# Optimization experiments

Hardware: AMD Instinct MI355X
Metric: run time of the kernel (lower is better)

Reference implementation:

```python
import jax, jax.numpy as jnp
import numpy as np

B, C, T = 8, 256, 8192
CALC, H = 256, 4
D = CALC // H  # head dim = 64
EPS = 1e-5


def setup_inputs() -> dict:
    key = jax.random.key(0)
    ks = jax.random.split(key, 5)
    return {
        "x": jax.random.normal(ks[0], (B, C, T), dtype=jnp.float32),
        "W_prenet": jax.random.normal(ks[1], (3 * CALC, C), dtype=jnp.float32) * 0.05,
        "W_proj": jax.random.normal(ks[2], (C, CALC), dtype=jnp.float32) * 0.05,
        "b_proj": jax.random.normal(ks[3], (C,), dtype=jnp.float32) * 0.05,
        "scale": jax.random.normal(ks[4], (1,), dtype=jnp.float32),
        "gamma": jnp.ones((C,), dtype=jnp.float32),
        "beta": jnp.zeros((C,), dtype=jnp.float32),
    }


def reference(x, W_prenet, W_proj, b_proj, scale, gamma, beta):
    residual = x
    # 1x1 conv prenet: [B, 3*CALC, T]
    h = jnp.einsum('oc,bct->bot', W_prenet, x)
    # split heads: channels grouped as H blocks of 3*D, then chunk into q/k/v of D each
    h = h.reshape(B, H, 3 * D, T)
    q = h[:, :, :D, :]            # [B,H,D,T]
    k = h[:, :, D:2 * D, :]
    v = h[:, :, 2 * D:, :]
    # softmax over time on keys (with the module's +1e-5 shift)
    k = jax.nn.softmax(k + EPS, axis=3)
    # keys @ values^T : [B,H,Dk,Dv]
    kv = jnp.einsum('bhdt,bhet->bhde', k, v)
    # kv^T @ queries  : [B,H,Dv,T]
    ctx = jnp.einsum('bhde,bhdt->bhet', kv, q)
    ctx = ctx.reshape(B, CALC, T)
    # 1x1 conv projection + bias
    out = jnp.einsum('oc,bct->bot', W_proj, ctx) + b_proj[None, :, None]
    out = scale * out  # learnable scalar gate
    # dropout is identity in eval mode
    out = out + residual
    # LayerNorm over channel axis with per-channel affine
    mean = jnp.mean(out, axis=1, keepdims=True)
    var = jnp.var(out, axis=1, keepdims=True)
    out = (out - mean) * jax.lax.rsqrt(var + EPS)
    out = out * gamma[None, :, None] + beta[None, :, None]
    return out
```

## Files before the change

### kernel.cpp

```cpp
#include <hip/hip_runtime.h>
#include <hip/hip_bf16.h>
#include <math.h>

#define BB 8
#define CC 256
#define TT 8192
#define EPSF 1e-5f

typedef short v8s __attribute__((ext_vector_type(8)));
typedef float v4f __attribute__((ext_vector_type(4)));

#define MFMA(a, b, c) __builtin_amdgcn_mfma_f32_16x16x32_bf16((a), (b), (c), 0, 0, 0)


#define OFF_WKV 0
#define OFF_WPJ 65536
#define OFF_UPART 98304
#define OFF_ZPART 4292608
#define OFF_KV 4423680
#define OFF_PT 4554752
#define OFF_MBF 4816896

__device__ __forceinline__ unsigned short f2bf(float f) {
  __hip_bfloat16 h = __float2bfloat16(f);
  return __builtin_bit_cast(unsigned short, h);
}
__device__ __forceinline__ float bf2f(unsigned short u) {
  return __bfloat162float(__builtin_bit_cast(__hip_bfloat16, u));
}
__device__ __forceinline__ unsigned int pack2(float lo, float hi) {
  return (unsigned int)f2bf(lo) | ((unsigned int)f2bf(hi) << 16);
}

__global__ void k0_pack(const float* __restrict__ Wpre,
                        const float* __restrict__ Wproj,
                        float* __restrict__ ws) {
  const int r = blockIdx.x;
  const int c = threadIdx.x;
  if (r < 512) {
    const int h = r >> 7, type = (r >> 6) & 1, d = r & 63;
    const int src = h * 192 + 64 + type * 64 + d;
    ((unsigned short*)(ws + OFF_WKV))[r * 256 + c] = f2bf(Wpre[(size_t)src * 256 + c]);
  } else {
    const int rr = r - 512;
    ((unsigned short*)(ws + OFF_WPJ))[rr * 256 + c] = f2bf(Wproj[(size_t)rr * 256 + c]);
  }
}

__global__ __launch_bounds__(512, 1) void k1_kv(const float* __restrict__ x,
                                                float* __restrict__ ws) {
  __shared__ unsigned short lds[74752];

  const int tid = threadIdx.x;
  const int w = tid >> 6, lane = tid & 63, q = lane >> 4, cl = lane & 15;
  const int h = w >> 1, thalf = w & 1;
  const int tw0 = thalf * 32;
  const int bi = blockIdx.x;
  const int b = bi >> 5, chunk = bi & 31;
  const int t0 = chunk * 256;
  const float* xb = x + (size_t)b * (CC * TT);
  const unsigned short* wk =
      (const unsigned short*)(ws + OFF_WKV) + (size_t)((h * 2 + 0) * 64) * 256;
  const unsigned short* wv =
      (const unsigned short*)(ws + OFF_WKV) + (size_t)((h * 2 + 1) * 64) * 256;
  unsigned short* evh = &lds[33792 + (h * 2) * 5120];
  unsigned short* ekw = evh + thalf * 5120;
  unsigned short* vbw = ekw + 2560;

  v4f Uacc[2][4];
#pragma unroll
  for (int i = 0; i < 2; ++i)
#pragma unroll
    for (int j = 0; j < 4; ++j) Uacc[i][j] = (v4f){0.f, 0.f, 0.f, 0.f};
  float zacc[4][4];
#pragma unroll
  for (int i = 0; i < 4; ++i)
#pragma unroll
    for (int j = 0; j < 4; ++j) zacc[i][j] = 0.f;

  const int c0 = (tid & 127) * 2;
  const int th = tid >> 7;
  const int cw = tid & 127;
  unsigned int* l32 = (unsigned int*)lds;

  {
    const float* xpA = xb + (size_t)c0 * TT + t0 + th * 16;
    const float* xpB = xpA + TT;
#pragma unroll
    for (int k = 0; k < 4; ++k) {
      const float4 va = reinterpret_cast<const float4*>(xpA)[k];
      const float4 vb4 = reinterpret_cast<const float4*>(xpB)[k];
      const int tb = th * 16 + k * 4;
      l32[(tb + 0) * 132 + cw] = pack2(va.x, vb4.x);
      l32[(tb + 1) * 132 + cw] = pack2(va.y, vb4.y);
      l32[(tb + 2) * 132 + cw] = pack2(va.z, vb4.z);
      l32[(tb + 3) * 132 + cw] = pack2(va.w, vb4.w);
    }
  }

  for (int sub = 0; sub < 4; ++sub) {
    const int cur = sub & 1;
    const unsigned short* xsr = &lds[cur * 16896];
    __syncthreads();

    v4f acc[4][2];

#pragma unroll
    for (int i = 0; i < 4; ++i)
#pragma unroll
      for (int j = 0; j < 2; ++j) acc[i][j] = (v4f){0.f, 0.f, 0.f, 0.f};
#pragma unroll
    for (int ks = 0; ks < 8; ++ks) {
      v8s af[4], bfu[2];
#pragma unroll
      for (int rt = 0; rt < 4; ++rt)
        af[rt] = *(const v8s*)(wk + (size_t)(rt * 16 + cl) * 256 + ks * 32 + q * 8);
#pragma unroll
      for (int ct = 0; ct < 2; ++ct)
        bfu[ct] = *(const v8s*)&xsr[(tw0 + ct * 16 + cl) * 264 + ks * 32 + q * 8];
#pragma unroll
      for (int rt = 0; rt < 4; ++rt)
#pragma unroll
        for (int ct = 0; ct < 2; ++ct)
          acc[rt][ct] = MFMA(af[rt], bfu[ct], acc[rt][ct]);
    }
#pragma unroll
    for (int rt = 0; rt < 4; ++rt)
#pragma unroll
      for (int ct = 0; ct < 2; ++ct)
#pragma unroll
        for (int reg = 0; reg < 4; ++reg) {
          const int row = rt * 16 + q * 4 + reg;
          const float e = __expf(acc[rt][ct][reg]);
          zacc[rt][reg] += e;
          ekw[row * 40 + ct * 16 + cl] = f2bf(e);
        }

#pragma unroll
    for (int i = 0; i < 4; ++i)
#pragma unroll
      for (int j = 0; j < 2; ++j) acc[i][j] = (v4f){0.f, 0.f, 0.f, 0.f};
#pragma unroll
    for (int ks = 0; ks < 8; ++ks) {
      v8s af[4], bfu[2];
#pragma unroll
      for (int rt = 0; rt < 4; ++rt)
        af[rt] = *(const v8s*)(wv + (size_t)(rt * 16 + cl) * 256 + ks * 32 + q * 8);
#pragma unroll
      for (int ct = 0; ct < 2; ++ct)
        bfu[ct] = *(const v8s*)&xsr[(tw0 + ct * 16 + cl) * 264 + ks * 32 + q * 8];
#pragma unroll
      for (int rt = 0; rt < 4; ++rt)
#pragma unroll
        for (int ct = 0; ct < 2; ++ct)
          acc[rt][ct] = MFMA(af[rt], bfu[ct], acc[rt][ct]);
    }
#pragma unroll
    for (int rt = 0; rt < 4; ++rt)
#pragma unroll
      for (int ct = 0; ct < 2; ++ct)
#pragma unroll
        for (int reg = 0; reg < 4; ++reg) {
          const int row = rt * 16 + q * 4 + reg;
          vbw[row * 40 + ct * 16 + cl] = f2bf(acc[rt][ct][reg]);
        }
    __syncthreads();

    float4 nxA[4], nxB[4];
    if (sub < 3) {
      const float* xpA = xb + (size_t)c0 * TT + (t0 + (sub + 1) * 64) + th * 16;
      const float* xpB = xpA + TT;
#pragma unroll
      for (int k = 0; k < 4; ++k) {
        nxA[k] = reinterpret_cast<const float4*>(xpA)[k];
        nxB[k] = reinterpret_cast<const float4*>(xpB)[k];
      }
    }

#pragma unroll
    for (int s = 0; s < 2; ++s) {
      const unsigned short* eks = evh + s * 5120;
      const unsigned short* vbs = eks + 2560;
      v8s afu[2], bfv[4];
#pragma unroll
      for (int ur = 0; ur < 2; ++ur)
        afu[ur] = *(const v8s*)&eks[(tw0 + ur * 16 + cl) * 40 + q * 8];
#pragma unroll
      for (int uc = 0; uc < 4; ++uc)
        bfv[uc] = *(const v8s*)&vbs[(uc * 16 + cl) * 40 + q * 8];
#pragma unroll
      for (int ur = 0; ur < 2; ++ur)
#pragma unroll
        for (int uc = 0; uc < 4; ++uc)
          Uacc[ur][uc] = MFMA(afu[ur], bfv[uc], Uacc[ur][uc]);
    }

    if (sub < 3) {
      unsigned int* xw = l32 + (cur ^ 1) * 8448;
#pragma unroll
      for (int k = 0; k < 4; ++k) {
        const int tb = th * 16 + k * 4;
        xw[(tb + 0) * 132 + cw] = pack2(nxA[k].x, nxB[k].x);
        xw[(tb + 1) * 132 + cw] = pack2(nxA[k].y, nxB[k].y);
        xw[(tb + 2) * 132 + cw] = pack2(nxA[k].z, nxB[k].z);
        xw[(tb + 3) * 132 + cw] = pack2(nxA[k].w, nxB[k].w);
      }
    }
  }

#pragma unroll
  for (int m = 1; m < 16; m <<= 1)
#pragma unroll
    for (int rt = 0; rt < 4; ++rt)
#pragma unroll
      for (int reg = 0; reg < 4; ++reg)
        zacc[rt][reg] += __shfl_xor(zacc[rt][reg], m, 64);
  if (cl == 0) {
    for (int rt = 0; rt < 4; ++rt)
      for (int reg = 0; reg < 4; ++reg)
        ws[OFF_ZPART + (size_t)bi * 512 + w * 64 + rt * 16 + q * 4 + reg] =
            zacc[rt][reg];
  }
  float* Up = ws + OFF_UPART + (size_t)bi * 16384 + h * 4096;
#pragma unroll
  for (int ur = 0; ur < 2; ++ur)
#pragma unroll
    for (int uc = 0; uc < 4; ++uc)
#pragma unroll
      for (int reg = 0; reg < 4; ++reg)
        Up[(tw0 + ur * 16 + q * 4 + reg) * 64 + uc * 16 + cl] =
            Uacc[ur][uc][reg];
}

__global__ void k2_reduce_kv(float* __restrict__ ws) {
  const int bi = blockIdx.x;
  const int bh = bi >> 4, j = bi & 15;
  const int b = bh >> 2, h = bh & 3;
  const int tid = threadIdx.x;

  __shared__ float zinv[64];
  if (tid < 64) {
    float z = 0.f;
#pragma unroll 4
    for (int cb = 0; cb < 32; ++cb) {
      const size_t base = OFF_ZPART + (size_t)(b * 32 + cb) * 512;
      z += ws[base + (h * 2 + 0) * 64 + tid] + ws[base + (h * 2 + 1) * 64 + tid];
    }
    zinv[tid] = 1.0f / z;
  }
  __syncthreads();

  const int idx = j * 256 + tid;
  const int d = idx >> 6;
  float s = 0.f;
#pragma unroll 4
  for (int cb = 0; cb < 32; ++cb)
    s += ws[OFF_UPART + (size_t)(b * 32 + cb) * 16384 + h * 4096 + idx];
  ws[OFF_KV + (size_t)(b * 4 + h) * 4096 + idx] = s * zinv[d];
}

__global__ void k3a_P(const float* __restrict__ Wpre, float* __restrict__ ws) {
  const int bi = blockIdx.x;
  const int b = bi >> 8, he = bi & 255;
  const int h = he >> 6, e = he & 63;
  const int c = threadIdx.x;
  const float* kvp = ws + OFF_KV + (size_t)(b * 4 + h) * 4096;
  float acc = 0.f;
#pragma unroll 8
  for (int d = 0; d < 64; ++d)
    acc += kvp[d * 64 + e] * Wpre[(size_t)(h * 192 + d) * 256 + c];
  ((unsigned short*)(ws + OFF_PT))[(size_t)b * 65536 + (size_t)c * 256 + he] =
      f2bf(acc);
}

__global__ __launch_bounds__(256, 2) void k3b_M(const float* __restrict__ scale,
                                                float* __restrict__ ws) {
  const int bi = blockIdx.x;
  const int b = bi >> 4, cg = (bi >> 2) & 3, rg = bi & 3;
  const int tid = threadIdx.x, w = tid >> 6, lane = tid & 63, q = lane >> 4,
            cl = lane & 15;
  const unsigned short* wpj = (const unsigned short*)(ws + OFF_WPJ);
  const unsigned short* pt =
      (const unsigned short*)(ws + OFF_PT) + (size_t)b * 65536;
  v4f acc[4];
#pragma unroll
  for (int j = 0; j < 4; ++j) acc[j] = (v4f){0.f, 0.f, 0.f, 0.f};
#pragma unroll
  for (int ks = 0; ks < 8; ++ks) {
    const v8s af = *(const v8s*)(wpj + (size_t)(rg * 64 + w * 16 + cl) * 256 +
                                 ks * 32 + q * 8);
    v8s bfu[4];
#pragma unroll
    for (int ct = 0; ct < 4; ++ct)
      bfu[ct] = *(const v8s*)(pt + (size_t)(cg * 64 + ct * 16 + cl) * 256 +
                              ks * 32 + q * 8);
#pragma unroll
    for (int ct = 0; ct < 4; ++ct) acc[ct] = MFMA(af, bfu[ct], acc[ct]);
  }
  const float s = scale[0];
  unsigned short* mbf = (unsigned short*)(ws + OFF_MBF);
#pragma unroll
  for (int ct = 0; ct < 4; ++ct)
#pragma unroll
    for (int reg = 0; reg < 4; ++reg) {
      const int o = rg * 64 + w * 16 + q * 4 + reg;
      const int c = cg * 64 + ct * 16 + cl;
      mbf[((size_t)b * 256 + o) * 256 + c] = f2bf(s * acc[ct][reg]);
    }
}

__global__ __launch_bounds__(256, 2) void k4_proj_ln(
    const float* __restrict__ x, const float* __restrict__ bproj,
    const float* __restrict__ scale, const float* __restrict__ gamma,
    const float* __restrict__ beta, const float* __restrict__ ws,
    float* __restrict__ out) {
  __shared__ unsigned short xs[32 * 264];
  __shared__ float red1[128], red2[128], muA[32], rsA[32];
  const int bi = blockIdx.x, b = bi >> 8, tc = bi & 255;
  const int tg0 = tc * 32;
  const int tid = threadIdx.x, w = tid >> 6, lane = tid & 63, q = lane >> 4,
            cl = lane & 15;
  const float* xb = x + (size_t)b * (CC * TT);

  {
    const int c0 = (tid & 127) * 2;
    const int th = tid >> 7;
    const float* xpA = xb + (size_t)c0 * TT + tg0 + th * 16;
    const float* xpB = xpA + TT;
    unsigned int* x32 = (unsigned int*)xs;
    const int cw = c0 >> 1;
#pragma unroll
    for (int k = 0; k < 4; ++k) {
      const float4 va = reinterpret_cast<const float4*>(xpA)[k];
      const float4 vb = reinterpret_cast<const float4*>(xpB)[k];
      const int tb = th * 16 + k * 4;
      x32[(tb + 0) * 132 + cw] = pack2(va.x, vb.x);
      x32[(tb + 1) * 132 + cw] = pack2(va.y, vb.y);
      x32[(tb + 2) * 132 + cw] = pack2(va.z, vb.z);
      x32[(tb + 3) * 132 + cw] = pack2(va.w, vb.w);
    }
  }
  __syncthreads();

  const unsigned short* mbf =
      (const unsigned short*)(ws + OFF_MBF) + (size_t)b * 65536;
  v4f acc[4][2];
#pragma unroll
  for (int i = 0; i < 4; ++i)
#pragma unroll
    for (int j = 0; j < 2; ++j) acc[i][j] = (v4f){0.f, 0.f, 0.f, 0.f};
#pragma unroll
  for (int ks = 0; ks < 8; ++ks) {
    v8s af[4], bfu[2];
#pragma unroll
    for (int rt = 0; rt < 4; ++rt)
      af[rt] = *(const v8s*)(mbf + (size_t)(w * 64 + rt * 16 + cl) * 256 +
                             ks * 32 + q * 8);
#pragma unroll
    for (int ct = 0; ct < 2; ++ct)
      bfu[ct] = *(const v8s*)&xs[(ct * 16 + cl) * 264 + ks * 32 + q * 8];
#pragma unroll
    for (int rt = 0; rt < 4; ++rt)
#pragma unroll
      for (int ct = 0; ct < 2; ++ct)
        acc[rt][ct] = MFMA(af[rt], bfu[ct], acc[rt][ct]);
  }

  const float s = scale[0];
#pragma unroll
  for (int rt = 0; rt < 4; ++rt)
#pragma unroll
    for (int reg = 0; reg < 4; ++reg) {
      const int o = w * 64 + rt * 16 + q * 4 + reg;
      const float sb = s * bproj[o];
#pragma unroll
      for (int ct = 0; ct < 2; ++ct) {
        const int tl = ct * 16 + cl;
        acc[rt][ct][reg] += sb + bf2f(xs[tl * 264 + o]);
      }
    }

#pragma unroll
  for (int ct = 0; ct < 2; ++ct) {
    float s1 = 0.f, s2 = 0.f;
#pragma unroll
    for (int rt = 0; rt < 4; ++rt)
#pragma unroll
      for (int reg = 0; reg < 4; ++reg) {
        const float v = acc[rt][ct][reg];
        s1 += v;
        s2 += v * v;
      }
    s1 += __shfl_xor(s1, 16, 64);
    s1 += __shfl_xor(s1, 32, 64);
    s2 += __shfl_xor(s2, 16, 64);
    s2 += __shfl_xor(s2, 32, 64);
    if (q == 0) {
      red1[w * 32 + ct * 16 + cl] = s1;
      red2[w * 32 + ct * 16 + cl] = s2;
    }
  }
  __syncthreads();
  if (tid < 32) {
    const float s1 = red1[tid] + red1[32 + tid] + red1[64 + tid] + red1[96 + tid];
    const float s2 = red2[tid] + red2[32 + tid] + red2[64 + tid] + red2[96 + tid];
    const float mu = s1 * (1.f / 256.f);
    const float var = s2 * (1.f / 256.f) - mu * mu;
    muA[tid] = mu;
    rsA[tid] = rsqrtf(var + EPSF);
  }
  __syncthreads();

  float* ob = out + (size_t)b * (CC * TT) + tg0;
#pragma unroll
  for (int rt = 0; rt < 4; ++rt)
#pragma unroll
    for (int reg = 0; reg < 4; ++reg) {
      const int o = w * 64 + rt * 16 + q * 4 + reg;
      const float g = gamma[o], bt = beta[o];
#pragma unroll
      for (int ct = 0; ct < 2; ++ct) {
        const int tl = ct * 16 + cl;
        ob[(size_t)o * TT + tl] = (acc[rt][ct][reg] - muA[tl]) * rsA[tl] * g + bt;
      }
    }
}

extern "C" void kernel_launch(void* const* d_in, const int* in_sizes, int n_in,
                              void* d_out, int out_size, void* d_ws,
                              size_t ws_size, hipStream_t stream) {
  (void)in_sizes; (void)n_in; (void)out_size; (void)ws_size;
  const float* x = (const float*)d_in[0];
  const float* Wpre = (const float*)d_in[1];
  const float* Wproj = (const float*)d_in[2];
  const float* bproj = (const float*)d_in[3];
  const float* scale = (const float*)d_in[4];
  const float* gamma = (const float*)d_in[5];
  const float* beta = (const float*)d_in[6];
  float* out = (float*)d_out;
  float* ws = (float*)d_ws;

  hipLaunchKernelGGL(k0_pack, dim3(768), dim3(256), 0, stream, Wpre, Wproj, ws);
  hipLaunchKernelGGL(k1_kv, dim3(256), dim3(512), 0, stream, x, ws);
  hipLaunchKernelGGL(k2_reduce_kv, dim3(512), dim3(256), 0, stream, ws);
  hipLaunchKernelGGL(k3a_P, dim3(BB * 256), dim3(256), 0, stream, Wpre, ws);
  hipLaunchKernelGGL(k3b_M, dim3(128), dim3(256), 0, stream, scale, ws);
  hipLaunchKernelGGL(k4_proj_ln, dim3(BB * 128 * 2), dim3(256), 0, stream, x,
                     bproj, scale, gamma, beta, ws, out);
}
```

Baseline: 254.1 us.

## Halve k1 time chunk and shrink LDS to fit two blocks per CU

The kv-accumulation kernel now processes 128 time steps per block instead of 256, launching 512 blocks. LDS drops from about 146KB to 65KB by removing x double-buffering and packing the exp(k) and v tiles into a dense 32-column XOR-swizzled layout, which also targets bank conflicts. Launch bounds allow two blocks per CU. In exchange it adds barriers, gives up the x double-buffer overlap, and doubles the partial sums the reduce kernel must read, with workspace offsets moved to fit.

```diff
diff --git a/kernel.cpp b/kernel.cpp
--- a/kernel.cpp
+++ b/kernel.cpp
@@ -16,10 +16,10 @@
 #define OFF_WKV 0
 #define OFF_WPJ 65536
 #define OFF_UPART 98304
-#define OFF_ZPART 4292608
-#define OFF_KV 4423680
-#define OFF_PT 4554752
-#define OFF_MBF 4816896
+#define OFF_ZPART 8486912
+#define OFF_KV 8749056
+#define OFF_PT 8880128
+#define OFF_MBF 9142272
 
 __device__ __forceinline__ unsigned short f2bf(float f) {
   __hip_bfloat16 h = __float2bfloat16(f);
@@ -30,6 +30,13 @@
 }
 __device__ __forceinline__ unsigned int pack2(float lo, float hi) {
   return (unsigned int)f2bf(lo) | ((unsigned int)f2bf(hi) << 16);
+}
+__device__ __forceinline__ int swz_w(int row, int col) {
+  return row * 32 + ((((col >> 3) ^ (row & 3) ^ ((row >> 2) & 3)) & 3) << 3) +
+         (col & 7);
+}
+__device__ __forceinline__ int swz_r(int row, int q) {
+  return row * 32 + (((q ^ (row & 3) ^ ((row >> 2) & 3)) & 3) << 3);
 }
 
 __global__ void k0_pack(const float* __restrict__ Wpre,
@@ -47,25 +54,24 @@
   }
 }
 
-__global__ __launch_bounds__(512, 1) void k1_kv(const float* __restrict__ x,
+__global__ __launch_bounds__(512, 2) void k1_kv(const float* __restrict__ x,
                                                 float* __restrict__ ws) {
-  __shared__ unsigned short lds[74752];
+  __shared__ unsigned short lds[33280];
 
   const int tid = threadIdx.x;
   const int w = tid >> 6, lane = tid & 63, q = lane >> 4, cl = lane & 15;
   const int h = w >> 1, thalf = w & 1;
   const int tw0 = thalf * 32;
   const int bi = blockIdx.x;
-  const int b = bi >> 5, chunk = bi & 31;
-  const int t0 = chunk * 256;
+  const int b = bi >> 6, chunk = bi & 63;
+  const int t0 = chunk * 128;
   const float* xb = x + (size_t)b * (CC * TT);
   const unsigned short* wk =
       (const unsigned short*)(ws + OFF_WKV) + (size_t)((h * 2 + 0) * 64) * 256;
   const unsigned short* wv =
       (const unsigned short*)(ws + OFF_WKV) + (size_t)((h * 2 + 1) * 64) * 256;
-  unsigned short* evh = &lds[33792 + (h * 2) * 5120];
-  unsigned short* ekw = evh + thalf * 5120;
-  unsigned short* vbw = ekw + 2560;
+  unsigned short* ekw = &lds[16896 + h * 4096 + thalf * 2048];
+  unsigned short* vbw_ = &lds[h * 4096 + thalf * 2048];
 
   v4f Uacc[2][4];
 #pragma unroll
@@ -98,9 +104,7 @@
     }
   }
 
-  for (int sub = 0; sub < 4; ++sub) {
-    const int cur = sub & 1;
-    const unsigned short* xsr = &lds[cur * 16896];
+  for (int sub = 0; sub < 2; ++sub) {
     __syncthreads();
 
     v4f acc[4][2];
@@ -117,7 +121,7 @@
         af[rt] = *(const v8s*)(wk + (size_t)(rt * 16 + cl) * 256 + ks * 32 + q * 8);
 #pragma unroll
       for (int ct = 0; ct < 2; ++ct)
-        bfu[ct] = *(const v8s*)&xsr[(tw0 + ct * 16 + cl) * 264 + ks * 32 + q * 8];
+        bfu[ct] = *(const v8s*)&lds[(tw0 + ct * 16 + cl) * 264 + ks * 32 + q * 8];
 #pragma unroll
       for (int rt = 0; rt < 4; ++rt)
 #pragma unroll
@@ -133,7 +137,7 @@
           const int row = rt * 16 + q * 4 + reg;
           const float e = __expf(acc[rt][ct][reg]);
           zacc[rt][reg] += e;
-          ekw[row * 40 + ct * 16 + cl] = f2bf(e);
+          ekw[swz_w(row, ct * 16 + cl)] = f2bf(e);
         }
 
 #pragma unroll
@@ -148,13 +152,15 @@
         af[rt] = *(const v8s*)(wv + (size_t)(rt * 16 + cl) * 256 + ks * 32 + q * 8);
 #pragma unroll
       for (int ct = 0; ct < 2; ++ct)
-        bfu[ct] = *(const v8s*)&xsr[(tw0 + ct * 16 + cl) * 264 + ks * 32 + q * 8];
+        bfu[ct] = *(const v8s*)&lds[(tw0 + ct * 16 + cl) * 264 + ks * 32 + q * 8];
 #pragma unroll
       for (int rt = 0; rt < 4; ++rt)
 #pragma unroll
         for (int ct = 0; ct < 2; ++ct)
           acc[rt][ct] = MFMA(af[rt], bfu[ct], acc[rt][ct]);
     }
+    __syncthreads();
+
 #pragma unroll
     for (int rt = 0; rt < 4; ++rt)
 #pragma unroll
@@ -162,13 +168,12 @@
 #pragma unroll
         for (int reg = 0; reg < 4; ++reg) {
           const int row = rt * 16 + q * 4 + reg;
-          vbw[row * 40 + ct * 16 + cl] = f2bf(acc[rt][ct][reg]);
+          vbw_[swz_w(row, ct * 16 + cl)] = f2bf(acc[rt][ct][reg]);
         }
-    __syncthreads();
 
     float4 nxA[4], nxB[4];
-    if (sub < 3) {
-      const float* xpA = xb + (size_t)c0 * TT + (t0 + (sub + 1) * 64) + th * 16;
+    if (sub == 0) {
+      const float* xpA = xb + (size_t)c0 * TT + (t0 + 64) + th * 16;
       const float* xpB = xpA + TT;
 #pragma unroll
       for (int k = 0; k < 4; ++k) {
@@ -176,18 +181,19 @@
         nxB[k] = reinterpret_cast<const float4*>(xpB)[k];
       }
     }
+    __syncthreads();
 
 #pragma unroll
     for (int s = 0; s < 2; ++s) {
-      const unsigned short* eks = evh + s * 5120;
-      const unsigned short* vbs = eks + 2560;
+      const unsigned short* eks = &lds[16896 + h * 4096 + s * 2048];
+      const unsigned short* vbs = &lds[h * 4096 + s * 2048];
       v8s afu[2], bfv[4];
 #pragma unroll
       for (int ur = 0; ur < 2; ++ur)
-        afu[ur] = *(const v8s*)&eks[(tw0 + ur * 16 + cl) * 40 + q * 8];
+        afu[ur] = *(const v8s*)&eks[swz_r(tw0 + ur * 16 + cl, q)];
 #pragma unroll
       for (int uc = 0; uc < 4; ++uc)
-        bfv[uc] = *(const v8s*)&vbs[(uc * 16 + cl) * 40 + q * 8];
+        bfv[uc] = *(const v8s*)&vbs[swz_r(uc * 16 + cl, q)];
 #pragma unroll
       for (int ur = 0; ur < 2; ++ur)
 #pragma unroll
@@ -195,15 +201,15 @@
           Uacc[ur][uc] = MFMA(afu[ur], bfv[uc], Uacc[ur][uc]);
     }
 
-    if (sub < 3) {
-      unsigned int* xw = l32 + (cur ^ 1) * 8448;
+    if (sub == 0) {
+      __syncthreads();
 #pragma unroll
       for (int k = 0; k < 4; ++k) {
         const int tb = th * 16 + k * 4;
-        xw[(tb + 0) * 132 + cw] = pack2(nxA[k].x, nxB[k].x);
-        xw[(tb + 1) * 132 + cw] = pack2(nxA[k].y, nxB[k].y);
-        xw[(tb + 2) * 132 + cw] = pack2(nxA[k].z, nxB[k].z);
-        xw[(tb + 3) * 132 + cw] = pack2(nxA[k].w, nxB[k].w);
+        l32[(tb + 0) * 132 + cw] = pack2(nxA[k].x, nxB[k].x);
+        l32[(tb + 1) * 132 + cw] = pack2(nxA[k].y, nxB[k].y);
+        l32[(tb + 2) * 132 + cw] = pack2(nxA[k].z, nxB[k].z);
+        l32[(tb + 3) * 132 + cw] = pack2(nxA[k].w, nxB[k].w);
       }
     }
   }
@@ -242,8 +248,8 @@
   if (tid < 64) {
     float z = 0.f;
 #pragma unroll 4
-    for (int cb = 0; cb < 32; ++cb) {
-      const size_t base = OFF_ZPART + (size_t)(b * 32 + cb) * 512;
+    for (int cb = 0; cb < 64; ++cb) {
+      const size_t base = OFF_ZPART + (size_t)(b * 64 + cb) * 512;
       z += ws[base + (h * 2 + 0) * 64 + tid] + ws[base + (h * 2 + 1) * 64 + tid];
     }
     zinv[tid] = 1.0f / z;
@@ -254,8 +260,8 @@
   const int d = idx >> 6;
   float s = 0.f;
 #pragma unroll 4
-  for (int cb = 0; cb < 32; ++cb)
-    s += ws[OFF_UPART + (size_t)(b * 32 + cb) * 16384 + h * 4096 + idx];
+  for (int cb = 0; cb < 64; ++cb)
+    s += ws[OFF_UPART + (size_t)(b * 64 + cb) * 16384 + h * 4096 + idx];
   ws[OFF_KV + (size_t)(b * 4 + h) * 4096 + idx] = s * zinv[d];
 }
 
@@ -441,7 +447,7 @@
   float* ws = (float*)d_ws;
 
   hipLaunchKernelGGL(k0_pack, dim3(768), dim3(256), 0, stream, Wpre, Wproj, ws);
-  hipLaunchKernelGGL(k1_kv, dim3(256), dim3(512), 0, stream, x, ws);
+  hipLaunchKernelGGL(k1_kv, dim3(512), dim3(512), 0, stream, x, ws);
   hipLaunchKernelGGL(k2_reduce_kv, dim3(512), dim3(256), 0, stream, ws);
   hipLaunchKernelGGL(k3a_P, dim3(BB * 256), dim3(256), 0, stream, Wpre, ws);
   hipLaunchKernelGGL(k3b_M, dim3(128), dim3(256), 0, stream, scale, ws);
```

Measured after the change: 289.3 us. +13.8%, slower.
